# Performance work log

Measured on AMD Instinct MI355X. Metric: run time of the kernel, lower is better.

The kernel has to match this reference:

```python
import jax, jax.numpy as jnp
import numpy as np

B, D, H, N, M, S = 64, 256, 512, 16384, 64, 3
EPS = 1e-4


def setup_inputs() -> dict:
    key = jax.random.key(0)
    ks = jax.random.split(key, 20)
    rn = lambda k, shape, sc=1.0: jax.random.normal(k, shape, dtype=jnp.float32) * sc
    z = lambda n: jnp.zeros((n,), jnp.float32)
    sc = 0.05
    return {
        "inp": rn(ks[0], (B, D)),
        "h_tm1": rn(ks[1], (B, H), 0.1),
        "c_tm1": rn(ks[2], (B, H), 0.1),
        "read_tm1": jax.nn.softmax(rn(ks[3], (B, N)), axis=-1),
        "write_tm1": jax.nn.softmax(rn(ks[4], (B, N)), axis=-1),
        "memory": rn(ks[5], (B, N, M), 0.1),
        "W_ih": rn(ks[6], (4 * H, D + M), sc), "b_ih": z(4 * H),
        "W_hh": rn(ks[7], (4 * H, H), sc), "b_hh": z(4 * H),
        "W_rk": rn(ks[8], (M, H), sc), "b_rk": z(M),
        "W_wk": rn(ks[9], (M, H), sc), "b_wk": z(M),
        "W_rc": rn(ks[10], (3, H), sc), "b_rc": z(3),
        "W_wc": rn(ks[11], (3, H), sc), "b_wc": z(3),
        "W_rs": rn(ks[12], (S, H), sc), "b_rs": z(S),
        "W_ws": rn(ks[13], (S, H), sc), "b_ws": z(S),
        "W_w": rn(ks[14], (2 * M, H), sc), "b_w": z(2 * M),
    }


def _head_params(h, Wk, bk, Wc, bc, Ws, bs):
    k = jnp.tanh(h @ Wk.T + bk)                 # [B, M] key
    c = h @ Wc.T + bc                           # [B, 3] beta/g/gamma raw
    s = jax.nn.softmax(h @ Ws.T + bs, axis=-1)  # [B, S] shift dist
    beta = jax.nn.relu(c[:, 0:1]) + EPS
    g = jax.nn.sigmoid(c[:, 1:2])
    gamma = jax.nn.relu(c[:, 2:3]) + 1.0 + EPS
    return k, s, beta, g, gamma


def _address(memory, w_tm1, k, s, beta, g, gamma):
    # content addressing: beta-scaled cosine similarity, softmax over slots
    dot = jnp.einsum('bm,bnm->bn', k, memory)                    # [B, N]
    nM = jnp.sqrt(jnp.sum(memory * memory, axis=-1)) + EPS       # [B, N]
    nk = jnp.sqrt(jnp.sum(k * k, axis=-1, keepdims=True)) + EPS  # [B, 1]
    content = jax.nn.softmax(beta * dot / (nM * nk), axis=-1)
    # interpolation with previous head
    inter = g * content + (1.0 - g) * w_tm1                      # [B, N]
    # circular shift conv: out[j] = sum_r s[r] * inter[(j + r - (S-1)) mod N]
    shifted = jnp.stack([jnp.roll(inter, S - 1 - r, axis=1) for r in range(S)], axis=-1)  # [B, N, S]
    conv = jnp.einsum('bns,bs->bn', shifted, s)
    # sharpening
    sharp = jnp.maximum(conv, 1e-8) ** gamma
    return sharp / jnp.sum(sharp, axis=1, keepdims=True)


def reference(inp, h_tm1, c_tm1, read_tm1, write_tm1, memory,
              W_ih, b_ih, W_hh, b_hh, W_rk, b_rk, W_wk, b_wk,
              W_rc, b_rc, W_wc, b_wc, W_rs, b_rs, W_ws, b_ws, W_w, b_w):
    # read head addressed from previous hidden state
    rk, rs, rbeta, rg, rgamma = _head_params(h_tm1, W_rk, b_rk, W_rc, b_rc, W_rs, b_rs)
    read_head = _address(memory, read_tm1, rk, rs, rbeta, rg, rgamma)
    M_read = jnp.einsum('bn,bnm->bm', read_head, memory)         # [B, M]
    # LSTMCell controller (torch gate order i, f, g, o)
    x = jnp.concatenate([inp, M_read], axis=1)
    gates = x @ W_ih.T + b_ih + h_tm1 @ W_hh.T + b_hh
    i, f, gg, o = jnp.split(gates, 4, axis=1)
    c_t = jax.nn.sigmoid(f) * c_tm1 + jax.nn.sigmoid(i) * jnp.tanh(gg)
    h_t = jax.nn.sigmoid(o) * jnp.tanh(c_t)
    # write head addressed from new hidden state
    wk, ws, wbeta, wg, wgamma = _head_params(h_t, W_wk, b_wk, W_wc, b_wc, W_ws, b_ws)
    write_head = _address(memory, write_tm1, wk, ws, wbeta, wg, wgamma)
    wa = h_t @ W_w.T + b_w
    e = jax.nn.sigmoid(wa[:, :M])                                # erase [B, M]
    a = wa[:, M:]                                                # add   [B, M]
    ww = write_head[:, :, None]                                  # [B, N, 1]
    M_out = memory * (1.0 - ww * e[:, None, :]) + ww * a[:, None, :]
    return (h_t, c_t, read_head, write_head, M_out)
```

## Files before the change

kernel.cpp:

```cpp
#include <hip/hip_runtime.h>
#include <math.h>

#define B_  64
#define D_  256
#define H_  512
#define N_  16384
#define M_  64
#define S_  3
#define EPS_ 1e-4f

__device__ __forceinline__ float sigmoidf_(float x) { return 1.0f / (1.0f + expf(-x)); }

template <bool WITH_W>
__global__ __launch_bounds__(256) void head_params_kernel(
    const float* __restrict__ h,
    const float* __restrict__ Wk, const float* __restrict__ bk,
    const float* __restrict__ Wc, const float* __restrict__ bc,
    const float* __restrict__ Ws, const float* __restrict__ bs,
    const float* __restrict__ Ww, const float* __restrict__ bw,
    float* __restrict__ k_out, float* __restrict__ nk_out,
    float* __restrict__ s_out,
    float* __restrict__ beta_out, float* __restrict__ g_out, float* __restrict__ gamma_out,
    float* __restrict__ e_out, float* __restrict__ a_out)
{
    const int b = blockIdx.x;
    const int tid = threadIdx.x;
    const int lane = tid & 63;
    const int wid = tid >> 6;
    __shared__ float raw[198];

    float h8[8];
    #pragma unroll
    for (int j = 0; j < 8; ++j) h8[j] = h[b * H_ + lane + 64 * j];

    const int count = WITH_W ? 198 : 70;
    for (int r = wid; r < count; r += 4) {
        const float* wrow;
        float bias;
        if (r < 64)       { wrow = Wk + r * H_;        bias = bk[r]; }
        else if (r < 67)  { wrow = Wc + (r - 64) * H_; bias = bc[r - 64]; }
        else if (r < 70)  { wrow = Ws + (r - 67) * H_; bias = bs[r - 67]; }
        else              { wrow = Ww + (r - 70) * H_; bias = bw[r - 70]; }
        float acc = 0.f;
        #pragma unroll
        for (int j = 0; j < 8; ++j) acc += wrow[lane + 64 * j] * h8[j];
        for (int off = 32; off >= 1; off >>= 1) acc += __shfl_xor(acc, off);
        if (lane == 0) raw[r] = acc + bias;
    }
    __syncthreads();

    if (tid < 64) {
        float kv = tanhf(raw[tid]);
        k_out[b * 64 + tid] = kv;
        float sq = kv * kv;
        for (int off = 32; off >= 1; off >>= 1) sq += __shfl_xor(sq, off);
        if (tid == 0) nk_out[b] = sqrtf(sq) + EPS_;
    } else if (tid == 64) {
        float c0 = raw[64], c1 = raw[65], c2 = raw[66];
        beta_out[b]  = fmaxf(c0, 0.f) + EPS_;
        g_out[b]     = sigmoidf_(c1);
        gamma_out[b] = fmaxf(c2, 0.f) + 1.f + EPS_;
    } else if (tid == 65) {
        float s0 = raw[67], s1 = raw[68], s2 = raw[69];
        float mx = fmaxf(s0, fmaxf(s1, s2));
        float e0 = expf(s0 - mx), e1 = expf(s1 - mx), e2 = expf(s2 - mx);
        float inv = 1.f / (e0 + e1 + e2);
        s_out[b * 3 + 0] = e0 * inv;
        s_out[b * 3 + 1] = e1 * inv;
        s_out[b * 3 + 2] = e2 * inv;
    }
    if (WITH_W && tid >= 128 && tid < 192) {
        int m = tid - 128;
        e_out[b * 64 + m] = sigmoidf_(raw[70 + m]);
        a_out[b * 64 + m] = raw[134 + m];
    }
}

template <int MODE>
__global__ __launch_bounds__(256) void score_kernel(
    const float* __restrict__ memory,
    const float* __restrict__ k,
    const float* __restrict__ beta_a,
    const float* __restrict__ nk_a,
    float* __restrict__ xout,
    float* __restrict__ nMbuf)
{
    const int tid = threadIdx.x;
    const int lane = tid & 63;
    const int wid = tid >> 6;
    const int grp = lane >> 4;
    const int m16 = lane & 15;
    const int b = blockIdx.x >> 8;
    const int nbase = (blockIdx.x & 255) * 64;
    const float4 k4 = ((const float4*)(k + b * 64))[m16];
    const float beta = beta_a[b], nk = nk_a[b];
    const int slot = wid * 4 + grp;
    const size_t bbase = (size_t)b * N_;
    #pragma unroll
    for (int it = 0; it < 4; ++it) {
        const int n = nbase + it * 16 + slot;
        const float4 m4 = ((const float4*)(memory + (bbase + n) * 64))[m16];
        float d  = m4.x * k4.x + m4.y * k4.y + m4.z * k4.z + m4.w * k4.w;
        float sq = 0.f;
        if (MODE == 0) sq = m4.x * m4.x + m4.y * m4.y + m4.z * m4.z + m4.w * m4.w;
        for (int off = 8; off >= 1; off >>= 1) {
            d += __shfl_xor(d, off);
            if (MODE == 0) sq += __shfl_xor(sq, off);
        }
        if (m16 == 0) {
            float nMv;
            if (MODE == 0) {
                nMv = sqrtf(sq) + EPS_;
                nMbuf[bbase + n] = nMv;
            } else {
                nMv = nMbuf[bbase + n];
            }
            xout[bbase + n] = beta * d / (nMv * nk);
        }
    }
}

__global__ __launch_bounds__(1024) void softmax_stats_kernel(
    const float* __restrict__ x,
    float* __restrict__ gmax_a, float* __restrict__ ginv_a)
{
    __shared__ float red[17];
    const int tid = threadIdx.x;
    const int b = blockIdx.x;
    const size_t base = (size_t)b * N_;
    const int wid = tid >> 6;

    float lx[16];
    float lmax = -1e30f;
    #pragma unroll
    for (int t = 0; t < 16; ++t) {
        lx[t] = x[base + t * 1024 + tid];
        lmax = fmaxf(lmax, lx[t]);
    }
    for (int off = 32; off >= 1; off >>= 1) lmax = fmaxf(lmax, __shfl_xor(lmax, off));
    if ((tid & 63) == 0) red[wid] = lmax;
    __syncthreads();
    if (tid == 0) {
        float v = red[0];
        for (int i = 1; i < 16; ++i) v = fmaxf(v, red[i]);
        red[16] = v;
    }
    __syncthreads();
    const float gmax = red[16];
    __syncthreads();

    float lsum = 0.f;
    #pragma unroll
    for (int t = 0; t < 16; ++t) lsum += expf(lx[t] - gmax);
    for (int off = 32; off >= 1; off >>= 1) lsum += __shfl_xor(lsum, off);
    if ((tid & 63) == 0) red[wid] = lsum;
    __syncthreads();
    if (tid == 0) {
        float v = 0.f;
        for (int i = 0; i < 16; ++i) v += red[i];
        gmax_a[b] = gmax;
        ginv_a[b] = 1.f / v;
    }
}

__global__ __launch_bounds__(256) void conv_sharp_kernel(
    const float* __restrict__ x,
    const float* __restrict__ w_tm1,
    const float* __restrict__ gmax_a, const float* __restrict__ ginv_a,
    const float* __restrict__ g_a, const float* __restrict__ gamma_a,
    const float* __restrict__ s_a,
    float* __restrict__ sharp, float* __restrict__ ssum)
{
    __shared__ float red[4];
    const int tid = threadIdx.x;
    const int b = blockIdx.x >> 6;
    const int n = (blockIdx.x & 63) * 256 + tid;
    const size_t base = (size_t)b * N_;
    const float gmax = gmax_a[b], ginv = ginv_a[b];
    const float g = g_a[b], gamma = gamma_a[b];
    const float s0 = s_a[b * 3 + 0], s1 = s_a[b * 3 + 1], s2 = s_a[b * 3 + 2];

    const int n1 = (n + N_ - 1) & (N_ - 1);
    const int n2 = (n + N_ - 2) & (N_ - 1);
    const float i0 = g * expf(x[base + n]  - gmax) * ginv + (1.f - g) * w_tm1[base + n];
    const float i1 = g * expf(x[base + n1] - gmax) * ginv + (1.f - g) * w_tm1[base + n1];
    const float i2 = g * expf(x[base + n2] - gmax) * ginv + (1.f - g) * w_tm1[base + n2];
    const float conv = s2 * i0 + s1 * i1 + s0 * i2;
    const float v = powf(fmaxf(conv, 1e-8f), gamma);
    sharp[base + n] = v;

    float lsum = v;
    for (int off = 32; off >= 1; off >>= 1) lsum += __shfl_xor(lsum, off);
    if ((tid & 63) == 0) red[tid >> 6] = lsum;
    __syncthreads();
    if (tid == 0) atomicAdd(&ssum[b], red[0] + red[1] + red[2] + red[3]);
}

__global__ __launch_bounds__(256) void mread_norm_kernel(
    const float* __restrict__ memory,
    const float* __restrict__ sharp,
    const float* __restrict__ ssum,
    float* __restrict__ rhead,
    float* __restrict__ M_read)
{
    const int tid = threadIdx.x;
    const int lane = tid & 63;
    const int wid = tid >> 6;
    const int grp = lane >> 4;
    const int m16 = lane & 15;
    const int b = blockIdx.x >> 6;
    const int nbase = (blockIdx.x & 63) * 256;
    const int slot = wid * 4 + grp;
    const size_t bbase = (size_t)b * N_;
    const float inv2 = 1.f / ssum[b];
    float4 acc = make_float4(0.f, 0.f, 0.f, 0.f);
    #pragma unroll 4
    for (int it = 0; it < 16; ++it) {
        const int n = nbase + it * 16 + slot;
        const float w = sharp[bbase + n] * inv2;
        const float4 m4 = ((const float4*)(memory + (bbase + n) * 64))[m16];
        if (m16 == 0) rhead[bbase + n] = w;
        acc.x += w * m4.x; acc.y += w * m4.y; acc.z += w * m4.z; acc.w += w * m4.w;
    }
    for (int off = 32; off >= 16; off >>= 1) {
        acc.x += __shfl_xor(acc.x, off);
        acc.y += __shfl_xor(acc.y, off);
        acc.z += __shfl_xor(acc.z, off);
        acc.w += __shfl_xor(acc.w, off);
    }
    __shared__ float4 part[64];
    if (lane < 16) part[wid * 16 + lane] = acc;
    __syncthreads();
    if (tid < 16) {
        float4 t = part[tid];
        for (int w = 1; w < 4; ++w) {
            const float4 p = part[w * 16 + tid];
            t.x += p.x; t.y += p.y; t.z += p.z; t.w += p.w;
        }
        atomicAdd(&M_read[b * 64 + tid * 4 + 0], t.x);
        atomicAdd(&M_read[b * 64 + tid * 4 + 1], t.y);
        atomicAdd(&M_read[b * 64 + tid * 4 + 2], t.z);
        atomicAdd(&M_read[b * 64 + tid * 4 + 3], t.w);
    }
}

__global__ __launch_bounds__(256) void gates_splitk_kernel(
    const float* __restrict__ inp,
    const float* __restrict__ M_read,
    const float* __restrict__ h_tm1,
    const float* __restrict__ W_ih,
    const float* __restrict__ W_hh,
    float* __restrict__ gates)
{
    __shared__ __align__(16) float Xsm[64][68];
    __shared__ __align__(16) float Wsm[64][68];
    const int tid = threadIdx.x;
    const int jb = blockIdx.x & 31;
    const int c  = blockIdx.x >> 5;
    const int j0 = jb * 64;

    #pragma unroll
    for (int i = 0; i < 4; ++i) {
        const int e = i * 256 + tid;
        const int row = e >> 4;
        const int c4 = e & 15;
        const float* xrow;
        if (c < 4)       xrow = inp    + row * 256 + c * 64;
        else if (c == 4) xrow = M_read + row * 64;
        else             xrow = h_tm1  + row * 512 + (c - 5) * 64;
        const float4 v = ((const float4*)xrow)[c4];
        const int kl = c4 * 4;
        Xsm[kl + 0][row] = v.x; Xsm[kl + 1][row] = v.y;
        Xsm[kl + 2][row] = v.z; Xsm[kl + 3][row] = v.w;
    }
    #pragma unroll
    for (int i = 0; i < 4; ++i) {
        const int e = i * 256 + tid;
        const int row = e >> 4;
        const int c4 = e & 15;
        const float* wrow;
        if (c < 5) wrow = W_ih + (j0 + row) * 320 + c * 64;
        else       wrow = W_hh + (j0 + row) * 512 + (c - 5) * 64;
        const float4 v = ((const float4*)wrow)[c4];
        const int kl = c4 * 4;
        Wsm[kl + 0][row] = v.x; Wsm[kl + 1][row] = v.y;
        Wsm[kl + 2][row] = v.z; Wsm[kl + 3][row] = v.w;
    }
    __syncthreads();

    const int tx = tid & 15, ty = tid >> 4;
    float acc[4][4] = {};
    #pragma unroll
    for (int k = 0; k < 64; ++k) {
        const float4 av = *((const float4*)&Xsm[k][ty * 4]);
        const float4 wv = *((const float4*)&Wsm[k][tx * 4]);
        acc[0][0] += av.x * wv.x; acc[0][1] += av.x * wv.y; acc[0][2] += av.x * wv.z; acc[0][3] += av.x * wv.w;
        acc[1][0] += av.y * wv.x; acc[1][1] += av.y * wv.y; acc[1][2] += av.y * wv.z; acc[1][3] += av.y * wv.w;
        acc[2][0] += av.z * wv.x; acc[2][1] += av.z * wv.y; acc[2][2] += av.z * wv.z; acc[2][3] += av.z * wv.w;
        acc[3][0] += av.w * wv.x; acc[3][1] += av.w * wv.y; acc[3][2] += av.w * wv.z; acc[3][3] += av.w * wv.w;
    }
    #pragma unroll
    for (int bi = 0; bi < 4; ++bi) {
        const int b = ty * 4 + bi;
        #pragma unroll
        for (int ji = 0; ji < 4; ++ji) {
            atomicAdd(&gates[b * 2048 + j0 + tx * 4 + ji], acc[bi][ji]);
        }
    }
}

__global__ __launch_bounds__(256) void lstm_kernel(
    const float* __restrict__ gates,
    const float* __restrict__ b_ih, const float* __restrict__ b_hh,
    const float* __restrict__ c_tm1,
    float* __restrict__ h_out, float* __restrict__ c_out)
{
    const int idx = blockIdx.x * 256 + threadIdx.x;
    const int b = idx >> 9, j = idx & 511;
    const float* gr = gates + b * 2048;
    const float i_ = sigmoidf_(gr[j]        + b_ih[j]        + b_hh[j]);
    const float f_ = sigmoidf_(gr[512 + j]  + b_ih[512 + j]  + b_hh[512 + j]);
    const float g_ = tanhf(   gr[1024 + j] + b_ih[1024 + j] + b_hh[1024 + j]);
    const float o_ = sigmoidf_(gr[1536 + j] + b_ih[1536 + j] + b_hh[1536 + j]);
    const float c = f_ * c_tm1[idx] + i_ * g_;
    c_out[idx] = c;
    h_out[idx] = o_ * tanhf(c);
}

__global__ __launch_bounds__(256) void mout_norm_kernel(
    const float* __restrict__ memory,
    const float* __restrict__ sharpw,
    const float* __restrict__ ssum_w,
    const float* __restrict__ e,
    const float* __restrict__ a,
    float* __restrict__ whead,
    float* __restrict__ M_out)
{
    const size_t total = (size_t)B_ * N_ * 16;
    const size_t stride = (size_t)gridDim.x * 256;
    for (size_t idx = (size_t)blockIdx.x * 256 + threadIdx.x; idx < total; idx += stride) {
        const size_t nlin = idx >> 4;
        const int m4 = (int)(idx & 15);
        const int b = (int)(nlin >> 14);
        const float w = sharpw[nlin] * (1.f / ssum_w[b]);
        const float4 ev = ((const float4*)(e + b * 64))[m4];
        const float4 av = ((const float4*)(a + b * 64))[m4];
        const float4 mv = ((const float4*)memory)[idx];
        if (m4 == 0) whead[nlin] = w;
        float4 o;
        o.x = mv.x * (1.f - w * ev.x) + w * av.x;
        o.y = mv.y * (1.f - w * ev.y) + w * av.y;
        o.z = mv.z * (1.f - w * ev.z) + w * av.z;
        o.w = mv.w * (1.f - w * ev.w) + w * av.w;
        ((float4*)M_out)[idx] = o;
    }
}

extern "C" void kernel_launch(void* const* d_in, const int* in_sizes, int n_in,
                              void* d_out, int out_size, void* d_ws, size_t ws_size,
                              hipStream_t stream)
{
    const float* inp       = (const float*)d_in[0];
    const float* h_tm1     = (const float*)d_in[1];
    const float* c_tm1     = (const float*)d_in[2];
    const float* read_tm1  = (const float*)d_in[3];
    const float* write_tm1 = (const float*)d_in[4];
    const float* memory    = (const float*)d_in[5];
    const float* W_ih = (const float*)d_in[6];  const float* b_ih = (const float*)d_in[7];
    const float* W_hh = (const float*)d_in[8];  const float* b_hh = (const float*)d_in[9];
    const float* W_rk = (const float*)d_in[10]; const float* b_rk = (const float*)d_in[11];
    const float* W_wk = (const float*)d_in[12]; const float* b_wk = (const float*)d_in[13];
    const float* W_rc = (const float*)d_in[14]; const float* b_rc = (const float*)d_in[15];
    const float* W_wc = (const float*)d_in[16]; const float* b_wc = (const float*)d_in[17];
    const float* W_rs = (const float*)d_in[18]; const float* b_rs = (const float*)d_in[19];
    const float* W_ws = (const float*)d_in[20]; const float* b_ws = (const float*)d_in[21];
    const float* W_w  = (const float*)d_in[22]; const float* b_w  = (const float*)d_in[23];

    float* out = (float*)d_out;
    float* h_out = out;
    float* c_out = out + 32768;
    float* rhead = out + 65536;
    float* whead = out + 65536 + 1048576;
    float* Mout  = out + 65536 + 2 * 1048576;

    float* x_r     = rhead;
    float* sharp_r = whead;
    float* x_w     = Mout;
    float* nMbuf   = Mout + (size_t)B_ * N_;
    float* sharp_w = whead;

    float* ws = (float*)d_ws;
    float* gates  = ws;
    float* M_read = ws + 131072;
    float* ssum_r = ws + 135168;
    float* ssum_w = ws + 135232;
    float* rk     = ws + 135296;
    float* wk     = ws + 139392;
    float* e_buf  = ws + 143488;
    float* a_buf  = ws + 147584;
    float* rs     = ws + 151680;
    float* wss    = ws + 151872;
    float* rbeta  = ws + 152064;
    float* rg     = ws + 152128;
    float* rgamma = ws + 152192;
    float* rnk    = ws + 152256;
    float* wbeta  = ws + 152320;
    float* wg     = ws + 152384;
    float* wgamma = ws + 152448;
    float* wnk    = ws + 152512;
    float* gmax_r = ws + 152576;
    float* ginv_r = ws + 152640;
    float* gmax_w = ws + 152704;
    float* ginv_w = ws + 152768;

    hipMemsetAsync(gates, 0, (131072 + 4096 + 64 + 64) * sizeof(float), stream);

    head_params_kernel<false><<<B_, 256, 0, stream>>>(
        h_tm1, W_rk, b_rk, W_rc, b_rc, W_rs, b_rs, nullptr, nullptr,
        rk, rnk, rs, rbeta, rg, rgamma, nullptr, nullptr);
    score_kernel<0><<<B_ * 256, 256, 0, stream>>>(memory, rk, rbeta, rnk, x_r, nMbuf);
    softmax_stats_kernel<<<B_, 1024, 0, stream>>>(x_r, gmax_r, ginv_r);
    conv_sharp_kernel<<<B_ * 64, 256, 0, stream>>>(
        x_r, read_tm1, gmax_r, ginv_r, rg, rgamma, rs, sharp_r, ssum_r);
    mread_norm_kernel<<<B_ * 64, 256, 0, stream>>>(memory, sharp_r, ssum_r, rhead, M_read);

    gates_splitk_kernel<<<13 * 32, 256, 0, stream>>>(inp, M_read, h_tm1, W_ih, W_hh, gates);
    lstm_kernel<<<128, 256, 0, stream>>>(gates, b_ih, b_hh, c_tm1, h_out, c_out);

    head_params_kernel<true><<<B_, 256, 0, stream>>>(
        h_out, W_wk, b_wk, W_wc, b_wc, W_ws, b_ws, W_w, b_w,
        wk, wnk, wss, wbeta, wg, wgamma, e_buf, a_buf);
    score_kernel<1><<<B_ * 256, 256, 0, stream>>>(memory, wk, wbeta, wnk, x_w, nMbuf);
    softmax_stats_kernel<<<B_, 1024, 0, stream>>>(x_w, gmax_w, ginv_w);
    conv_sharp_kernel<<<B_ * 64, 256, 0, stream>>>(
        x_w, write_tm1, gmax_w, ginv_w, wg, wgamma, wss, sharp_w, ssum_w);
    mout_norm_kernel<<<16384, 256, 0, stream>>>(
        memory, sharp_w, ssum_w, e_buf, a_buf, whead, Mout);
}
```

Before: 817.7 us.

## Fuse softmax stats into score kernel and M_read into conv kernel

Drops the max-subtraction softmax pass: the score kernel now writes exp(x) directly and accumulates per-batch sums with atomics, which removes the separate softmax_stats launch. The conv kernel stages interpolated values in shared memory with a halo and computes the M_read accumulation in the same pass, so the separate mread_norm kernel goes away. Normalisation of the read head moves into the write score kernel and of M_read into the gates kernel. Skipping the max subtraction relies on beta*cosine staying small enough not to overflow exp. The head_params kernel also runs 512 threads instead of 256.

```diff
diff --git a/kernel.cpp b/kernel.cpp
--- a/kernel.cpp
+++ b/kernel.cpp
@@ -12,7 +12,7 @@
 __device__ __forceinline__ float sigmoidf_(float x) { return 1.0f / (1.0f + expf(-x)); }
 
 template <bool WITH_W>
-__global__ __launch_bounds__(256) void head_params_kernel(
+__global__ __launch_bounds__(512) void head_params_kernel(
     const float* __restrict__ h,
     const float* __restrict__ Wk, const float* __restrict__ bk,
     const float* __restrict__ Wc, const float* __restrict__ bc,
@@ -34,7 +34,7 @@
     for (int j = 0; j < 8; ++j) h8[j] = h[b * H_ + lane + 64 * j];
 
     const int count = WITH_W ? 198 : 70;
-    for (int r = wid; r < count; r += 4) {
+    for (int r = wid; r < count; r += 8) {
         const float* wrow;
         float bias;
         if (r < 64)       { wrow = Wk + r * H_;        bias = bk[r]; }
@@ -77,14 +77,19 @@
 }
 
 template <int MODE>
-__global__ __launch_bounds__(256) void score_kernel(
+__global__ __launch_bounds__(256) void scoreE_kernel(
     const float* __restrict__ memory,
     const float* __restrict__ k,
     const float* __restrict__ beta_a,
     const float* __restrict__ nk_a,
-    float* __restrict__ xout,
-    float* __restrict__ nMbuf)
-{
+    float* __restrict__ Eout,
+    float* __restrict__ nMbuf,
+    float* __restrict__ sumE,
+    const float* __restrict__ sharp_prev,
+    const float* __restrict__ ssum_prev,
+    float* __restrict__ head_prev)
+{
+    __shared__ float red[4];
     const int tid = threadIdx.x;
     const int lane = tid & 63;
     const int wid = tid >> 6;
@@ -96,6 +101,15 @@
     const float beta = beta_a[b], nk = nk_a[b];
     const int slot = wid * 4 + grp;
     const size_t bbase = (size_t)b * N_;
+
+    if (MODE == 1) {
+        if (tid < 64) {
+            const float rinv = 1.f / ssum_prev[b];
+            head_prev[bbase + nbase + tid] = sharp_prev[bbase + nbase + tid] * rinv;
+        }
+    }
+
+    float lsum = 0.f;
     #pragma unroll
     for (int it = 0; it < 4; ++it) {
         const int n = nbase + it * 16 + slot;
@@ -115,141 +129,106 @@
             } else {
                 nMv = nMbuf[bbase + n];
             }
-            xout[bbase + n] = beta * d / (nMv * nk);
-        }
-    }
-}
-
-__global__ __launch_bounds__(1024) void softmax_stats_kernel(
-    const float* __restrict__ x,
-    float* __restrict__ gmax_a, float* __restrict__ ginv_a)
-{
-    __shared__ float red[17];
-    const int tid = threadIdx.x;
-    const int b = blockIdx.x;
-    const size_t base = (size_t)b * N_;
-    const int wid = tid >> 6;
-
-    float lx[16];
-    float lmax = -1e30f;
-    #pragma unroll
-    for (int t = 0; t < 16; ++t) {
-        lx[t] = x[base + t * 1024 + tid];
-        lmax = fmaxf(lmax, lx[t]);
-    }
-    for (int off = 32; off >= 1; off >>= 1) lmax = fmaxf(lmax, __shfl_xor(lmax, off));
-    if ((tid & 63) == 0) red[wid] = lmax;
+            const float E = expf(beta * d / (nMv * nk));
+            Eout[bbase + n] = E;
+            lsum += E;
+        }
+    }
+    for (int off = 32; off >= 1; off >>= 1) lsum += __shfl_xor(lsum, off);
+    if (lane == 0) red[wid] = lsum;
     __syncthreads();
-    if (tid == 0) {
-        float v = red[0];
-        for (int i = 1; i < 16; ++i) v = fmaxf(v, red[i]);
-        red[16] = v;
-    }
-    __syncthreads();
-    const float gmax = red[16];
-    __syncthreads();
-
-    float lsum = 0.f;
-    #pragma unroll
-    for (int t = 0; t < 16; ++t) lsum += expf(lx[t] - gmax);
-    for (int off = 32; off >= 1; off >>= 1) lsum += __shfl_xor(lsum, off);
-    if ((tid & 63) == 0) red[wid] = lsum;
-    __syncthreads();
-    if (tid == 0) {
-        float v = 0.f;
-        for (int i = 0; i < 16; ++i) v += red[i];
-        gmax_a[b] = gmax;
-        ginv_a[b] = 1.f / v;
-    }
-}
-
-__global__ __launch_bounds__(256) void conv_sharp_kernel(
-    const float* __restrict__ x,
+    if (tid == 0) atomicAdd(&sumE[b], red[0] + red[1] + red[2] + red[3]);
+}
+
+template <bool WITH_MREAD>
+__global__ __launch_bounds__(256) void conv_kernel(
+    const float* __restrict__ memory,
+    const float* __restrict__ E,
     const float* __restrict__ w_tm1,
-    const float* __restrict__ gmax_a, const float* __restrict__ ginv_a,
+    const float* __restrict__ sumE,
     const float* __restrict__ g_a, const float* __restrict__ gamma_a,
     const float* __restrict__ s_a,
-    float* __restrict__ sharp, float* __restrict__ ssum)
-{
+    float* __restrict__ sharp,
+    float* __restrict__ ssum,
+    float* __restrict__ M_read_un)
+{
+    __shared__ float inter_sm[258];
+    __shared__ float sharp_sm[256];
     __shared__ float red[4];
+    __shared__ float4 part[64];
     const int tid = threadIdx.x;
     const int b = blockIdx.x >> 6;
-    const int n = (blockIdx.x & 63) * 256 + tid;
+    const int nbase = (blockIdx.x & 63) * 256;
     const size_t base = (size_t)b * N_;
-    const float gmax = gmax_a[b], ginv = ginv_a[b];
+    const float ginv = 1.f / sumE[b];
     const float g = g_a[b], gamma = gamma_a[b];
     const float s0 = s_a[b * 3 + 0], s1 = s_a[b * 3 + 1], s2 = s_a[b * 3 + 2];
 
-    const int n1 = (n + N_ - 1) & (N_ - 1);
-    const int n2 = (n + N_ - 2) & (N_ - 1);
-    const float i0 = g * expf(x[base + n]  - gmax) * ginv + (1.f - g) * w_tm1[base + n];
-    const float i1 = g * expf(x[base + n1] - gmax) * ginv + (1.f - g) * w_tm1[base + n1];
-    const float i2 = g * expf(x[base + n2] - gmax) * ginv + (1.f - g) * w_tm1[base + n2];
-    const float conv = s2 * i0 + s1 * i1 + s0 * i2;
-    const float v = powf(fmaxf(conv, 1e-8f), gamma);
-    sharp[base + n] = v;
-
-    float lsum = v;
-    for (int off = 32; off >= 1; off >>= 1) lsum += __shfl_xor(lsum, off);
-    if ((tid & 63) == 0) red[tid >> 6] = lsum;
+    {
+        const int n = nbase + tid;
+        inter_sm[tid + 2] = g * E[base + n] * ginv + (1.f - g) * w_tm1[base + n];
+        if (tid < 2) {
+            const int nh = (nbase + N_ - 2 + tid) & (N_ - 1);
+            inter_sm[tid] = g * E[base + nh] * ginv + (1.f - g) * w_tm1[base + nh];
+        }
+    }
+    __syncthreads();
+    {
+        const float conv = s2 * inter_sm[tid + 2] + s1 * inter_sm[tid + 1]
+                         + s0 * inter_sm[tid];
+        const float v = powf(fmaxf(conv, 1e-8f), gamma);
+        sharp_sm[tid] = v;
+        sharp[base + nbase + tid] = v;
+        float ls = v;
+        for (int off = 32; off >= 1; off >>= 1) ls += __shfl_xor(ls, off);
+        if ((tid & 63) == 0) red[tid >> 6] = ls;
+    }
     __syncthreads();
     if (tid == 0) atomicAdd(&ssum[b], red[0] + red[1] + red[2] + red[3]);
-}
-
-__global__ __launch_bounds__(256) void mread_norm_kernel(
-    const float* __restrict__ memory,
-    const float* __restrict__ sharp,
-    const float* __restrict__ ssum,
-    float* __restrict__ rhead,
-    float* __restrict__ M_read)
-{
-    const int tid = threadIdx.x;
-    const int lane = tid & 63;
-    const int wid = tid >> 6;
-    const int grp = lane >> 4;
-    const int m16 = lane & 15;
-    const int b = blockIdx.x >> 6;
-    const int nbase = (blockIdx.x & 63) * 256;
-    const int slot = wid * 4 + grp;
-    const size_t bbase = (size_t)b * N_;
-    const float inv2 = 1.f / ssum[b];
-    float4 acc = make_float4(0.f, 0.f, 0.f, 0.f);
-    #pragma unroll 4
-    for (int it = 0; it < 16; ++it) {
-        const int n = nbase + it * 16 + slot;
-        const float w = sharp[bbase + n] * inv2;
-        const float4 m4 = ((const float4*)(memory + (bbase + n) * 64))[m16];
-        if (m16 == 0) rhead[bbase + n] = w;
-        acc.x += w * m4.x; acc.y += w * m4.y; acc.z += w * m4.z; acc.w += w * m4.w;
-    }
-    for (int off = 32; off >= 16; off >>= 1) {
-        acc.x += __shfl_xor(acc.x, off);
-        acc.y += __shfl_xor(acc.y, off);
-        acc.z += __shfl_xor(acc.z, off);
-        acc.w += __shfl_xor(acc.w, off);
-    }
-    __shared__ float4 part[64];
-    if (lane < 16) part[wid * 16 + lane] = acc;
-    __syncthreads();
-    if (tid < 16) {
-        float4 t = part[tid];
-        for (int w = 1; w < 4; ++w) {
-            const float4 p = part[w * 16 + tid];
-            t.x += p.x; t.y += p.y; t.z += p.z; t.w += p.w;
-        }
-        atomicAdd(&M_read[b * 64 + tid * 4 + 0], t.x);
-        atomicAdd(&M_read[b * 64 + tid * 4 + 1], t.y);
-        atomicAdd(&M_read[b * 64 + tid * 4 + 2], t.z);
-        atomicAdd(&M_read[b * 64 + tid * 4 + 3], t.w);
+
+    if (WITH_MREAD) {
+        const int lane = tid & 63;
+        const int wid = tid >> 6;
+        const int grp = lane >> 4;
+        const int m16 = lane & 15;
+        const int slot = wid * 4 + grp;
+        float4 acc = make_float4(0.f, 0.f, 0.f, 0.f);
+        #pragma unroll 4
+        for (int it = 0; it < 16; ++it) {
+            const int nl = it * 16 + slot;
+            const float w = sharp_sm[nl];
+            const float4 m4 = ((const float4*)(memory + (base + nbase + nl) * 64))[m16];
+            acc.x += w * m4.x; acc.y += w * m4.y; acc.z += w * m4.z; acc.w += w * m4.w;
+        }
+        for (int off = 32; off >= 16; off >>= 1) {
+            acc.x += __shfl_xor(acc.x, off);
+            acc.y += __shfl_xor(acc.y, off);
+            acc.z += __shfl_xor(acc.z, off);
+            acc.w += __shfl_xor(acc.w, off);
+        }
+        if (lane < 16) part[wid * 16 + lane] = acc;
+        __syncthreads();
+        if (tid < 16) {
+            float4 t = part[tid];
+            for (int w2 = 1; w2 < 4; ++w2) {
+                const float4 q = part[w2 * 16 + tid];
+                t.x += q.x; t.y += q.y; t.z += q.z; t.w += q.w;
+            }
+            atomicAdd(&M_read_un[b * 64 + tid * 4 + 0], t.x);
+            atomicAdd(&M_read_un[b * 64 + tid * 4 + 1], t.y);
+            atomicAdd(&M_read_un[b * 64 + tid * 4 + 2], t.z);
+            atomicAdd(&M_read_un[b * 64 + tid * 4 + 3], t.w);
+        }
     }
 }
 
 __global__ __launch_bounds__(256) void gates_splitk_kernel(
     const float* __restrict__ inp,
-    const float* __restrict__ M_read,
+    const float* __restrict__ M_read_un,
     const float* __restrict__ h_tm1,
     const float* __restrict__ W_ih,
     const float* __restrict__ W_hh,
+    const float* __restrict__ ssum_r,
     float* __restrict__ gates)
 {
     __shared__ __align__(16) float Xsm[64][68];
@@ -265,10 +244,14 @@
         const int row = e >> 4;
         const int c4 = e & 15;
         const float* xrow;
-        if (c < 4)       xrow = inp    + row * 256 + c * 64;
-        else if (c == 4) xrow = M_read + row * 64;
-        else             xrow = h_tm1  + row * 512 + (c - 5) * 64;
-        const float4 v = ((const float4*)xrow)[c4];
+        if (c < 4)       xrow = inp       + row * 256 + c * 64;
+        else if (c == 4) xrow = M_read_un + row * 64;
+        else             xrow = h_tm1     + row * 512 + (c - 5) * 64;
+        float4 v = ((const float4*)xrow)[c4];
+        if (c == 4) {
+            const float sc = 1.f / ssum_r[row];
+            v.x *= sc; v.y *= sc; v.z *= sc; v.w *= sc;
+        }
         const int kl = c4 * 4;
         Xsm[kl + 0][row] = v.x; Xsm[kl + 1][row] = v.y;
         Xsm[kl + 2][row] = v.z; Xsm[kl + 3][row] = v.w;
@@ -383,57 +366,55 @@
     float* whead = out + 65536 + 1048576;
     float* Mout  = out + 65536 + 2 * 1048576;
 
-    float* x_r     = rhead;
+    float* E_r     = rhead;
     float* sharp_r = whead;
-    float* x_w     = Mout;
+    float* E_w     = Mout;
     float* nMbuf   = Mout + (size_t)B_ * N_;
     float* sharp_w = whead;
 
     float* ws = (float*)d_ws;
-    float* gates  = ws;
-    float* M_read = ws + 131072;
-    float* ssum_r = ws + 135168;
-    float* ssum_w = ws + 135232;
-    float* rk     = ws + 135296;
-    float* wk     = ws + 139392;
-    float* e_buf  = ws + 143488;
-    float* a_buf  = ws + 147584;
-    float* rs     = ws + 151680;
-    float* wss    = ws + 151872;
-    float* rbeta  = ws + 152064;
-    float* rg     = ws + 152128;
-    float* rgamma = ws + 152192;
-    float* rnk    = ws + 152256;
-    float* wbeta  = ws + 152320;
-    float* wg     = ws + 152384;
-    float* wgamma = ws + 152448;
-    float* wnk    = ws + 152512;
-    float* gmax_r = ws + 152576;
-    float* ginv_r = ws + 152640;
-    float* gmax_w = ws + 152704;
-    float* ginv_w = ws + 152768;
-
-    hipMemsetAsync(gates, 0, (131072 + 4096 + 64 + 64) * sizeof(float), stream);
-
-    head_params_kernel<false><<<B_, 256, 0, stream>>>(
+    float* gates     = ws;
+    float* M_read_un = ws + 131072;
+    float* sum_r     = ws + 135168;
+    float* sum_w     = ws + 135232;
+    float* ssum_r    = ws + 135296;
+    float* ssum_w    = ws + 135360;
+    float* rk        = ws + 135424;
+    float* wk        = ws + 139520;
+    float* e_buf     = ws + 143616;
+    float* a_buf     = ws + 147712;
+    float* rs        = ws + 151808;
+    float* wss       = ws + 152000;
+    float* rbeta     = ws + 152192;
+    float* rg        = ws + 152256;
+    float* rgamma    = ws + 152320;
+    float* rnk       = ws + 152384;
+    float* wbeta     = ws + 152448;
+    float* wg        = ws + 152512;
+    float* wgamma    = ws + 152576;
+    float* wnk       = ws + 152640;
+
+    hipMemsetAsync(gates, 0, 135424 * sizeof(float), stream);
+
+    head_params_kernel<false><<<B_, 512, 0, stream>>>(
         h_tm1, W_rk, b_rk, W_rc, b_rc, W_rs, b_rs, nullptr, nullptr,
         rk, rnk, rs, rbeta, rg, rgamma, nullptr, nullptr);
-    score_kernel<0><<<B_ * 256, 256, 0, stream>>>(memory, rk, rbeta, rnk, x_r, nMbuf);
-    softmax_stats_kernel<<<B_, 1024, 0, stream>>>(x_r, gmax_r, ginv_r);
-    conv_sharp_kernel<<<B_ * 64, 256, 0, stream>>>(
-        x_r, read_tm1, gmax_r, ginv_r, rg, rgamma, rs, sharp_r, ssum_r);
-    mread_norm_kernel<<<B_ * 64, 256, 0, stream>>>(memory, sharp_r, ssum_r, rhead, M_read);
-
-    gates_splitk_kernel<<<13 * 32, 256, 0, stream>>>(inp, M_read, h_tm1, W_ih, W_hh, gates);
+    scoreE_kernel<0><<<B_ * 256, 256, 0, stream>>>(
+        memory, rk, rbeta, rnk, E_r, nMbuf, sum_r, nullptr, nullptr, nullptr);
+    conv_kernel<true><<<B_ * 64, 256, 0, stream>>>(
+        memory, E_r, read_tm1, sum_r, rg, rgamma, rs, sharp_r, ssum_r, M_read_un);
+
+    gates_splitk_kernel<<<13 * 32, 256, 0, stream>>>(
+        inp, M_read_un, h_tm1, W_ih, W_hh, ssum_r, gates);
     lstm_kernel<<<128, 256, 0, stream>>>(gates, b_ih, b_hh, c_tm1, h_out, c_out);
 
-    head_params_kernel<true><<<B_, 256, 0, stream>>>(
+    head_params_kernel<true><<<B_, 512, 0, stream>>>(
         h_out, W_wk, b_wk, W_wc, b_wc, W_ws, b_ws, W_w, b_w,
         wk, wnk, wss, wbeta, wg, wgamma, e_buf, a_buf);
-    score_kernel<1><<<B_ * 256, 256, 0, stream>>>(memory, wk, wbeta, wnk, x_w, nMbuf);
-    softmax_stats_kernel<<<B_, 1024, 0, stream>>>(x_w, gmax_w, ginv_w);
-    conv_sharp_kernel<<<B_ * 64, 256, 0, stream>>>(
-        x_w, write_tm1, gmax_w, ginv_w, wg, wgamma, wss, sharp_w, ssum_w);
+    scoreE_kernel<1><<<B_ * 256, 256, 0, stream>>>(
+        memory, wk, wbeta, wnk, E_w, nMbuf, sum_w, sharp_r, ssum_r, rhead);
+    conv_kernel<false><<<B_ * 64, 256, 0, stream>>>(
+        nullptr, E_w, write_tm1, sum_w, wg, wgamma, wss, sharp_w, ssum_w, nullptr);
     mout_norm_kernel<<<16384, 256, 0, stream>>>(
         memory, sharp_w, ssum_w, e_buf, a_buf, whead, Mout);
 }
```

Measured after the change: 953.0 us. 1.17x slower.
